# Kernel tuning notes

Measured on AMD Instinct MI355X. Metric: run time of the kernel, lower is better.

The kernel has to match this reference:

```python
import jax, jax.numpy as jnp
import numpy as np


def setup_inputs() -> dict:
    key = jax.random.key(0)
    k1, k2 = jax.random.split(key)
    x = jax.random.normal(k1, (2, 8, 32, 32, 64), dtype=jnp.float32)
    gamma = jax.random.normal(k2, (1,), dtype=jnp.float32)
    return {"x": x, "gamma": gamma}


def reference(x, gamma):
    # x: (B, D, H, W, C) -> flatten spatial dims to N = D*H*W
    B, D, H, W, C = x.shape
    N = D * H * W
    q = x.reshape(B, N, C)                       # proj_query (B, N, C)
    # energy = Q @ Q^T : (B, N, N) self-similarity over spatial positions
    energy = jnp.einsum('bnc,bmc->bnm', q, q)
    attn = jax.nn.softmax(energy, axis=-1)       # softmax over last axis (keras default)
    out = jnp.einsum('bnm,bmc->bnc', attn, q)    # attention @ Q -> (B, N, C)
    out = out.reshape(B, D, H, W, C)
    return gamma * out + x
```

## Files before the change

kernel.cpp:

```cpp
#include <hip/hip_runtime.h>
#include <hip/hip_bf16.h>

typedef __attribute__((ext_vector_type(8))) short bf16x8;
typedef __attribute__((ext_vector_type(16))) float f32x16;
typedef __attribute__((ext_vector_type(4))) int int4v;

#define NB 2
#define NN 8192
#define NC 64
#define LOG2E 1.44269504088896340736f
#define INV_LOG2E 0.69314718055994530942f
#define MAXNORM_BOUND 16.0f
#define KSTRIDE 68
#define SKIP_THRESH -110.0f
#define LSPLITC 3
#define SPLIT (1 << LSPLITC)
#define KT_PER (128 / SPLIT)

union I4 { int4v v; unsigned long long u[2]; };

__device__ __forceinline__ bf16x8 lds_ld16(const __hip_bfloat16* p) {
    union { bf16x8 v; unsigned long long u[2]; } r;
    r.u[0] = *(const unsigned long long*)(p);
    r.u[1] = *(const unsigned long long*)(p + 4);
    return r.v;
}

__global__ __launch_bounds__(256) void prep_kernel(
        const float* __restrict__ x,
        __hip_bfloat16* __restrict__ qb) {
    const int i = blockIdx.x * 256 + threadIdx.x;
    const float* src = x + ((size_t)i << 3);
    float4 f0 = *(const float4*)(src);
    float4 f1 = *(const float4*)(src + 4);
    __align__(16) __hip_bfloat16 h[8];
    h[0] = __float2bfloat16(f0.x); h[1] = __float2bfloat16(f0.y);
    h[2] = __float2bfloat16(f0.z); h[3] = __float2bfloat16(f0.w);
    h[4] = __float2bfloat16(f1.x); h[5] = __float2bfloat16(f1.y);
    h[6] = __float2bfloat16(f1.z); h[7] = __float2bfloat16(f1.w);
    *(int4v*)(qb + ((size_t)i << 3)) = *(const int4v*)h;
}

__global__ __launch_bounds__(512, 4) void attn_kernel(
        const __hip_bfloat16* __restrict__ qb,
        float* __restrict__ opart,
        float* __restrict__ lpart) {
    __shared__ __hip_bfloat16 Ks[512][KSTRIDE];

    const int blk   = blockIdx.x;
    const int chunk = blk & (SPLIT - 1);
    const int qw    = (blk >> LSPLITC) & 31;
    const int b     = blk >> (5 + LSPLITC);
    const int q0    = qw << 8;
    const int tid  = threadIdx.x;
    const int wave = tid >> 6;
    const int lane = tid & 63;
    const int n5   = lane & 31;
    const int h    = lane >> 5;
    const int q0w  = q0 + (wave << 5);

    const __hip_bfloat16* kvptr = qb + ((size_t)b << 19);

    const int srow = tid >> 3;
    const int scb  = (tid & 7) << 3;

    const __hip_bfloat16* qrow = kvptr + (((size_t)(q0w + n5)) << 6);
    bf16x8 Qf[4];
#pragma unroll
    for (int step = 0; step < 4; ++step)
        Qf[step] = *(const bf16x8*)(qrow + (step << 4) + (h << 3));

    float mb2, thr;
    {
        float s = 0.f;
#pragma unroll
        for (int step = 0; step < 4; ++step)
#pragma unroll
            for (int j = 0; j < 8; ++j) {
                float f = __uint_as_float(((unsigned)(unsigned short)Qf[step][j]) << 16);
                s += f * f;
            }
        s += __shfl_xor(s, 32);
        mb2 = sqrtf(s) * (MAXNORM_BOUND * LOG2E);
        thr = (SKIP_THRESH + mb2) * INV_LOG2E;
    }

    f32x16 O0 = (f32x16)(0.f), O1 = (f32x16)(0.f);
    float lp = 0.f;
    bool wkeep = false;

    const int kb0 = (chunk * KT_PER) << 6;

#define STAGE(BASEK) do {                                                         \
        I4 g[8];                                                                  \
        _Pragma("unroll")                                                         \
        for (int j = 0; j < 8; ++j)                                               \
            g[j].v = *(const int4v*)(kvptr +                                      \
                (((size_t)((BASEK) + srow + (j << 6))) << 6) + scb);              \
        _Pragma("unroll")                                                         \
        for (int j = 0; j < 8; ++j) {                                             \
            *(unsigned long long*)(&Ks[srow + (j << 6)][scb])     = g[j].u[0];    \
            *(unsigned long long*)(&Ks[srow + (j << 6)][scb + 4]) = g[j].u[1];    \
        }                                                                         \
    } while (0)

#define SLABPHASE() do {                                                          \
        unsigned km = 0;                                                          \
        _Pragma("clang loop unroll(disable)")                                     \
        for (int t = 0; t < 8; ++t) {                                             \
            f32x16 ST0 = (f32x16)(0.f), ST1 = (f32x16)(0.f);                      \
            _Pragma("unroll")                                                     \
            for (int step = 0; step < 4; ++step) {                                \
                bf16x8 a0 = lds_ld16(&Ks[(t << 6) + n5][(step << 4) + (h << 3)]); \
                bf16x8 a1 = lds_ld16(&Ks[(t << 6) + 32 + n5][(step << 4) + (h << 3)]); \
                ST0 = __builtin_amdgcn_mfma_f32_32x32x16_bf16(a0, Qf[step], ST0, 0, 0, 0); \
                ST1 = __builtin_amdgcn_mfma_f32_32x32x16_bf16(a1, Qf[step], ST1, 0, 0, 0); \
            }                                                                     \
            float mx[8];                                                          \
            _Pragma("unroll")                                                     \
            for (int r = 0; r < 8; ++r)                                           \
                mx[r] = fmaxf(fmaxf(ST0[r], ST0[r + 8]),                          \
                              fmaxf(ST1[r], ST1[r + 8]));                         \
            _Pragma("unroll")                                                     \
            for (int d = 4; d; d >>= 1)                                           \
                _Pragma("unroll")                                                 \
                for (int r = 0; r < d; ++r) mx[r] = fmaxf(mx[r], mx[r + d]);      \
            if (__ballot(mx[0] >= thr) != 0ull) km |= (1u << t);                  \
        }                                                                         \
        while (km) {                                                              \
            const int t = __builtin_ctz(km);                                      \
            km &= km - 1;                                                         \
            wkeep = true;                                                         \
            f32x16 ST0 = (f32x16)(0.f), ST1 = (f32x16)(0.f);                      \
            _Pragma("unroll")                                                     \
            for (int step = 0; step < 4; ++step) {                                \
                bf16x8 a0 = lds_ld16(&Ks[(t << 6) + n5][(step << 4) + (h << 3)]); \
                bf16x8 a1 = lds_ld16(&Ks[(t << 6) + 32 + n5][(step << 4) + (h << 3)]); \
                ST0 = __builtin_amdgcn_mfma_f32_32x32x16_bf16(a0, Qf[step], ST0, 0, 0, 0); \
                ST1 = __builtin_amdgcn_mfma_f32_32x32x16_bf16(a1, Qf[step], ST1, 0, 0, 0); \
            }                                                                     \
            bf16x8 bP[4];                                                         \
            _Pragma("unroll")                                                     \
            for (int s = 0; s < 4; ++s) {                                         \
                _Pragma("unroll")                                                 \
                for (int j = 0; j < 8; ++j) {                                     \
                    const float sv = (s < 2) ? ST0[((s & 1) << 3) + j]            \
                                             : ST1[((s & 1) << 3) + j];           \
                    float p = __builtin_amdgcn_exp2f(fmaf(sv, LOG2E, -mb2));      \
                    lp += p;                                                      \
                    bP[s][j] = __builtin_bit_cast(short, __float2bfloat16(p));    \
                }                                                                 \
            }                                                                     \
            \
            _Pragma("unroll")                                                     \
            for (int s = 0; s < 4; ++s) {                                         \
                bf16x8 a0, a1;                                                    \
                _Pragma("unroll")                                                 \
                for (int j = 0; j < 8; ++j) {                                     \
                    const int kap = (t << 6) + (s << 4) + (h << 2)                \
                                    + (j & 3) + ((j >> 2) << 3);                  \
                    a0[j] = __builtin_bit_cast(short, Ks[kap][n5]);               \
                    a1[j] = __builtin_bit_cast(short, Ks[kap][32 + n5]);          \
                }                                                                 \
                O0 = __builtin_amdgcn_mfma_f32_32x32x16_bf16(a0, bP[s], O0, 0, 0, 0); \
                O1 = __builtin_amdgcn_mfma_f32_32x32x16_bf16(a1, bP[s], O1, 0, 0, 0); \
            }                                                                     \
        }                                                                         \
    } while (0)

    STAGE(kb0);
    __syncthreads();
    SLABPHASE();

    __syncthreads();
    STAGE(kb0 + 512);
    __syncthreads();
    SLABPHASE();

#undef SLABPHASE
#undef STAGE

    float lsum = lp + __shfl_xor(lp, 32);
    if (h == 0)
        lpart[(chunk << 14) + (b << 13) + q0w + n5] = lsum;

    if (wkeep) {
        float* orow = opart + ((size_t)chunk << 20) +
                      (((size_t)((b << 13) + q0w + n5)) << 6);
#pragma unroll
        for (int g4 = 0; g4 < 4; ++g4) {
            float4 f0 = make_float4(O0[(g4 << 2)], O0[(g4 << 2) + 1],
                                    O0[(g4 << 2) + 2], O0[(g4 << 2) + 3]);
            *(float4*)(orow + (g4 << 3) + (h << 2)) = f0;
            float4 f1 = make_float4(O1[(g4 << 2)], O1[(g4 << 2) + 1],
                                    O1[(g4 << 2) + 2], O1[(g4 << 2) + 3]);
            *(float4*)(orow + 32 + (g4 << 3) + (h << 2)) = f1;
        }
    }
}

__global__ __launch_bounds__(256) void finalize_kernel(
        const float* __restrict__ x,
        const float* __restrict__ gamma_p,
        const float* __restrict__ opart,
        const float* __restrict__ lpart,
        float* __restrict__ out) {
    const int i4 = blockIdx.x * 256 + threadIdx.x;
    const size_t e = (size_t)i4 << 2;
    const int rowg = i4 >> 4;

    float l = 0.f;
    float4 o = make_float4(0.f, 0.f, 0.f, 0.f);
#pragma unroll
    for (int c = 0; c < SPLIT; ++c) {
        const float lc = lpart[(c << 14) + rowg];
        l += lc;
        if (lc != 0.f) {
            float4 t = *(const float4*)(opart + ((size_t)c << 20) + e);
            o.x += t.x; o.y += t.y; o.z += t.z; o.w += t.w;
        }
    }
    const float inv = 1.0f / l;
    const float gm = gamma_p[0];
    float4 xin = *(const float4*)(x + e);
    float4 r;
    r.x = gm * (o.x * inv) + xin.x;
    r.y = gm * (o.y * inv) + xin.y;
    r.z = gm * (o.z * inv) + xin.z;
    r.w = gm * (o.w * inv) + xin.w;
    *(float4*)(out + e) = r;
}

extern "C" void kernel_launch(void* const* d_in, const int* in_sizes, int n_in,
                              void* d_out, int out_size, void* d_ws, size_t ws_size,
                              hipStream_t stream) {
    const float* x     = (const float*)d_in[0];
    const float* gamma = (const float*)d_in[1];
    float* out = (float*)d_out;

    __hip_bfloat16* qb = (__hip_bfloat16*)d_ws;
    float* opart = (float*)((char*)d_ws + (size_t)2 * 1024 * 1024);
    float* lpart = opart + ((size_t)SPLIT << 20);

    prep_kernel<<<512, 256, 0, stream>>>(x, qb);
    attn_kernel<<<NB * 32 * SPLIT, 512, 0, stream>>>(qb, opart, lpart);
    finalize_kernel<<<(NB * NN * NC / 4) / 256, 256, 0, stream>>>(x, gamma, opart, lpart, out);
}
```

Baseline: 93.35 us.

## Process two 32-query subtiles per wave to reuse K fragments from LDS

Each wave now handles 64 queries (two 32-row groups) instead of 32, so every K fragment loaded from LDS feeds four MFMAs instead of two, and the grid is halved. The intent is to cut LDS traffic and global K staging per query. The cost is more registers (launch bounds relaxed to 2 blocks per CU), half as many blocks, and coarser skip decisions, since a tile is now kept if either query group needs it.

```diff
diff --git a/kernel.cpp b/kernel.cpp
--- a/kernel.cpp
+++ b/kernel.cpp
@@ -41,7 +41,7 @@
     *(int4v*)(qb + ((size_t)i << 3)) = *(const int4v*)h;
 }
 
-__global__ __launch_bounds__(512, 4) void attn_kernel(
+__global__ __launch_bounds__(512, 2) void attn_kernel(
         const __hip_bfloat16* __restrict__ qb,
         float* __restrict__ opart,
         float* __restrict__ lpart) {
@@ -49,44 +49,52 @@
 
     const int blk   = blockIdx.x;
     const int chunk = blk & (SPLIT - 1);
-    const int qw    = (blk >> LSPLITC) & 31;
-    const int b     = blk >> (5 + LSPLITC);
-    const int q0    = qw << 8;
+    const int qw    = (blk >> LSPLITC) & 15;
+    const int b     = blk >> (4 + LSPLITC);
+    const int q0    = qw << 9;
     const int tid  = threadIdx.x;
     const int wave = tid >> 6;
     const int lane = tid & 63;
     const int n5   = lane & 31;
     const int h    = lane >> 5;
-    const int q0w  = q0 + (wave << 5);
+    const int q0w  = q0 + (wave << 6);
 
     const __hip_bfloat16* kvptr = qb + ((size_t)b << 19);
 
     const int srow = tid >> 3;
     const int scb  = (tid & 7) << 3;
 
-    const __hip_bfloat16* qrow = kvptr + (((size_t)(q0w + n5)) << 6);
-    bf16x8 Qf[4];
-#pragma unroll
-    for (int step = 0; step < 4; ++step)
-        Qf[step] = *(const bf16x8*)(qrow + (step << 4) + (h << 3));
-
-    float mb2, thr;
+    const __hip_bfloat16* qrowA = kvptr + (((size_t)(q0w + n5)) << 6);
+    const __hip_bfloat16* qrowB = kvptr + (((size_t)(q0w + 32 + n5)) << 6);
+    bf16x8 Qf[4], Qg[4];
+#pragma unroll
+    for (int step = 0; step < 4; ++step) {
+        Qf[step] = *(const bf16x8*)(qrowA + (step << 4) + (h << 3));
+        Qg[step] = *(const bf16x8*)(qrowB + (step << 4) + (h << 3));
+    }
+
+    float mb2A, thrA, mb2B, thrB;
     {
-        float s = 0.f;
+        float sA = 0.f, sB = 0.f;
 #pragma unroll
         for (int step = 0; step < 4; ++step)
 #pragma unroll
             for (int j = 0; j < 8; ++j) {
-                float f = __uint_as_float(((unsigned)(unsigned short)Qf[step][j]) << 16);
-                s += f * f;
+                float fA = __uint_as_float(((unsigned)(unsigned short)Qf[step][j]) << 16);
+                float fB = __uint_as_float(((unsigned)(unsigned short)Qg[step][j]) << 16);
+                sA += fA * fA; sB += fB * fB;
             }
-        s += __shfl_xor(s, 32);
-        mb2 = sqrtf(s) * (MAXNORM_BOUND * LOG2E);
-        thr = (SKIP_THRESH + mb2) * INV_LOG2E;
-    }
-
-    f32x16 O0 = (f32x16)(0.f), O1 = (f32x16)(0.f);
-    float lp = 0.f;
+        sA += __shfl_xor(sA, 32);
+        sB += __shfl_xor(sB, 32);
+        mb2A = sqrtf(sA) * (MAXNORM_BOUND * LOG2E);
+        thrA = (SKIP_THRESH + mb2A) * INV_LOG2E;
+        mb2B = sqrtf(sB) * (MAXNORM_BOUND * LOG2E);
+        thrB = (SKIP_THRESH + mb2B) * INV_LOG2E;
+    }
+
+    f32x16 OA0 = (f32x16)(0.f), OA1 = (f32x16)(0.f);
+    f32x16 OB0 = (f32x16)(0.f), OB1 = (f32x16)(0.f);
+    float lpA = 0.f, lpB = 0.f;
     bool wkeep = false;
 
     const int kb0 = (chunk * KT_PER) << 6;
@@ -104,54 +112,70 @@
         }                                                                         \
     } while (0)
 
+#define EXPPV(ST0, ST1, MB2, BP, LP) do {                                         \
+        _Pragma("unroll")                                                         \
+        for (int s = 0; s < 4; ++s) {                                             \
+            _Pragma("unroll")                                                     \
+            for (int j = 0; j < 8; ++j) {                                         \
+                const float sv = (s < 2) ? ST0[((s & 1) << 3) + j]                \
+                                         : ST1[((s & 1) << 3) + j];               \
+                float p = __builtin_amdgcn_exp2f(fmaf(sv, LOG2E, -(MB2)));        \
+                LP += p;                                                          \
+                BP[s][j] = __builtin_bit_cast(short, __float2bfloat16(p));        \
+            }                                                                     \
+        }                                                                         \
+    } while (0)
+
 #define SLABPHASE() do {                                                          \
         unsigned km = 0;                                                          \
         _Pragma("clang loop unroll(disable)")                                     \
         for (int t = 0; t < 8; ++t) {                                             \
-            f32x16 ST0 = (f32x16)(0.f), ST1 = (f32x16)(0.f);                      \
+            f32x16 SA0 = (f32x16)(0.f), SA1 = (f32x16)(0.f);                      \
+            f32x16 SB0 = (f32x16)(0.f), SB1 = (f32x16)(0.f);                      \
             _Pragma("unroll")                                                     \
             for (int step = 0; step < 4; ++step) {                                \
                 bf16x8 a0 = lds_ld16(&Ks[(t << 6) + n5][(step << 4) + (h << 3)]); \
                 bf16x8 a1 = lds_ld16(&Ks[(t << 6) + 32 + n5][(step << 4) + (h << 3)]); \
-                ST0 = __builtin_amdgcn_mfma_f32_32x32x16_bf16(a0, Qf[step], ST0, 0, 0, 0); \
-                ST1 = __builtin_amdgcn_mfma_f32_32x32x16_bf16(a1, Qf[step], ST1, 0, 0, 0); \
-            }                                                                     \
-            float mx[8];                                                          \
-            _Pragma("unroll")                                                     \
-            for (int r = 0; r < 8; ++r)                                           \
-                mx[r] = fmaxf(fmaxf(ST0[r], ST0[r + 8]),                          \
-                              fmaxf(ST1[r], ST1[r + 8]));                         \
+                SA0 = __builtin_amdgcn_mfma_f32_32x32x16_bf16(a0, Qf[step], SA0, 0, 0, 0); \
+                SA1 = __builtin_amdgcn_mfma_f32_32x32x16_bf16(a1, Qf[step], SA1, 0, 0, 0); \
+                SB0 = __builtin_amdgcn_mfma_f32_32x32x16_bf16(a0, Qg[step], SB0, 0, 0, 0); \
+                SB1 = __builtin_amdgcn_mfma_f32_32x32x16_bf16(a1, Qg[step], SB1, 0, 0, 0); \
+            }                                                                     \
+            float mxA[8], mxB[8];                                                 \
+            _Pragma("unroll")                                                     \
+            for (int r = 0; r < 8; ++r) {                                         \
+                mxA[r] = fmaxf(fmaxf(SA0[r], SA0[r + 8]), fmaxf(SA1[r], SA1[r + 8])); \
+                mxB[r] = fmaxf(fmaxf(SB0[r], SB0[r + 8]), fmaxf(SB1[r], SB1[r + 8])); \
+            }                                                                     \
             _Pragma("unroll")                                                     \
             for (int d = 4; d; d >>= 1)                                           \
                 _Pragma("unroll")                                                 \
-                for (int r = 0; r < d; ++r) mx[r] = fmaxf(mx[r], mx[r + d]);      \
-            if (__ballot(mx[0] >= thr) != 0ull) km |= (1u << t);                  \
+                for (int r = 0; r < d; ++r) {                                     \
+                    mxA[r] = fmaxf(mxA[r], mxA[r + d]);                           \
+                    mxB[r] = fmaxf(mxB[r], mxB[r + d]);                           \
+                }                                                                 \
+            const bool kp = (mxA[0] >= thrA) || (mxB[0] >= thrB);                 \
+            if (__ballot(kp) != 0ull) km |= (1u << t);                            \
         }                                                                         \
         while (km) {                                                              \
             const int t = __builtin_ctz(km);                                      \
             km &= km - 1;                                                         \
             wkeep = true;                                                         \
-            f32x16 ST0 = (f32x16)(0.f), ST1 = (f32x16)(0.f);                      \
+            f32x16 SA0 = (f32x16)(0.f), SA1 = (f32x16)(0.f);                      \
+            f32x16 SB0 = (f32x16)(0.f), SB1 = (f32x16)(0.f);                      \
             _Pragma("unroll")                                                     \
             for (int step = 0; step < 4; ++step) {                                \
                 bf16x8 a0 = lds_ld16(&Ks[(t << 6) + n5][(step << 4) + (h << 3)]); \
                 bf16x8 a1 = lds_ld16(&Ks[(t << 6) + 32 + n5][(step << 4) + (h << 3)]); \
-                ST0 = __builtin_amdgcn_mfma_f32_32x32x16_bf16(a0, Qf[step], ST0, 0, 0, 0); \
-                ST1 = __builtin_amdgcn_mfma_f32_32x32x16_bf16(a1, Qf[step], ST1, 0, 0, 0); \
-            }                                                                     \
-            bf16x8 bP[4];                                                         \
-            _Pragma("unroll")                                                     \
-            for (int s = 0; s < 4; ++s) {                                         \
-                _Pragma("unroll")                                                 \
-                for (int j = 0; j < 8; ++j) {                                     \
-                    const float sv = (s < 2) ? ST0[((s & 1) << 3) + j]            \
-                                             : ST1[((s & 1) << 3) + j];           \
-                    float p = __builtin_amdgcn_exp2f(fmaf(sv, LOG2E, -mb2));      \
-                    lp += p;                                                      \
-                    bP[s][j] = __builtin_bit_cast(short, __float2bfloat16(p));    \
-                }                                                                 \
-            }                                                                     \
-            \
+                SA0 = __builtin_amdgcn_mfma_f32_32x32x16_bf16(a0, Qf[step], SA0, 0, 0, 0); \
+                SA1 = __builtin_amdgcn_mfma_f32_32x32x16_bf16(a1, Qf[step], SA1, 0, 0, 0); \
+                SB0 = __builtin_amdgcn_mfma_f32_32x32x16_bf16(a0, Qg[step], SB0, 0, 0, 0); \
+                SB1 = __builtin_amdgcn_mfma_f32_32x32x16_bf16(a1, Qg[step], SB1, 0, 0, 0); \
+            }                                                                     \
+            bf16x8 bPA[4], bPB[4];                                                \
+            EXPPV(SA0, SA1, mb2A, bPA, lpA);                                      \
+            EXPPV(SB0, SB1, mb2B, bPB, lpB);                                      \
+                            \
             _Pragma("unroll")                                                     \
             for (int s = 0; s < 4; ++s) {                                         \
                 bf16x8 a0, a1;                                                    \
@@ -162,8 +186,10 @@
                     a0[j] = __builtin_bit_cast(short, Ks[kap][n5]);               \
                     a1[j] = __builtin_bit_cast(short, Ks[kap][32 + n5]);          \
                 }                                                                 \
-                O0 = __builtin_amdgcn_mfma_f32_32x32x16_bf16(a0, bP[s], O0, 0, 0, 0); \
-                O1 = __builtin_amdgcn_mfma_f32_32x32x16_bf16(a1, bP[s], O1, 0, 0, 0); \
+                OA0 = __builtin_amdgcn_mfma_f32_32x32x16_bf16(a0, bPA[s], OA0, 0, 0, 0); \
+                OA1 = __builtin_amdgcn_mfma_f32_32x32x16_bf16(a1, bPA[s], OA1, 0, 0, 0); \
+                OB0 = __builtin_amdgcn_mfma_f32_32x32x16_bf16(a0, bPB[s], OB0, 0, 0, 0); \
+                OB1 = __builtin_amdgcn_mfma_f32_32x32x16_bf16(a1, bPB[s], OB1, 0, 0, 0); \
             }                                                                     \
         }                                                                         \
     } while (0)
@@ -178,23 +204,35 @@
     SLABPHASE();
 
 #undef SLABPHASE
+#undef EXPPV
 #undef STAGE
 
-    float lsum = lp + __shfl_xor(lp, 32);
-    if (h == 0)
-        lpart[(chunk << 14) + (b << 13) + q0w + n5] = lsum;
+    float lsA = lpA + __shfl_xor(lpA, 32);
+    float lsB = lpB + __shfl_xor(lpB, 32);
+    if (h == 0) {
+        lpart[(chunk << 14) + (b << 13) + q0w + n5]      = lsA;
+        lpart[(chunk << 14) + (b << 13) + q0w + 32 + n5] = lsB;
+    }
 
     if (wkeep) {
-        float* orow = opart + ((size_t)chunk << 20) +
-                      (((size_t)((b << 13) + q0w + n5)) << 6);
+        float* orowA = opart + ((size_t)chunk << 20) +
+                       (((size_t)((b << 13) + q0w + n5)) << 6);
+        float* orowB = opart + ((size_t)chunk << 20) +
+                       (((size_t)((b << 13) + q0w + 32 + n5)) << 6);
 #pragma unroll
         for (int g4 = 0; g4 < 4; ++g4) {
-            float4 f0 = make_float4(O0[(g4 << 2)], O0[(g4 << 2) + 1],
-                                    O0[(g4 << 2) + 2], O0[(g4 << 2) + 3]);
-            *(float4*)(orow + (g4 << 3) + (h << 2)) = f0;
-            float4 f1 = make_float4(O1[(g4 << 2)], O1[(g4 << 2) + 1],
-                                    O1[(g4 << 2) + 2], O1[(g4 << 2) + 3]);
-            *(float4*)(orow + 32 + (g4 << 3) + (h << 2)) = f1;
+            *(float4*)(orowA + (g4 << 3) + (h << 2)) =
+                make_float4(OA0[(g4 << 2)], OA0[(g4 << 2) + 1],
+                            OA0[(g4 << 2) + 2], OA0[(g4 << 2) + 3]);
+            *(float4*)(orowA + 32 + (g4 << 3) + (h << 2)) =
+                make_float4(OA1[(g4 << 2)], OA1[(g4 << 2) + 1],
+                            OA1[(g4 << 2) + 2], OA1[(g4 << 2) + 3]);
+            *(float4*)(orowB + (g4 << 3) + (h << 2)) =
+                make_float4(OB0[(g4 << 2)], OB0[(g4 << 2) + 1],
+                            OB0[(g4 << 2) + 2], OB0[(g4 << 2) + 3]);
+            *(float4*)(orowB + 32 + (g4 << 3) + (h << 2)) =
+                make_float4(OB1[(g4 << 2)], OB1[(g4 << 2) + 1],
+                            OB1[(g4 << 2) + 2], OB1[(g4 << 2) + 3]);
         }
     }
 }
@@ -243,6 +281,6 @@
     float* lpart = opart + ((size_t)SPLIT << 20);
 
     prep_kernel<<<512, 256, 0, stream>>>(x, qb);
-    attn_kernel<<<NB * 32 * SPLIT, 512, 0, stream>>>(qb, opart, lpart);
+    attn_kernel<<<NB * 16 * SPLIT, 512, 0, stream>>>(qb, opart, lpart);
     finalize_kernel<<<(NB * NN * NC / 4) / 256, 256, 0, stream>>>(x, gamma, opart, lpart, out);
 }
```

Result: slower. 98.93 us (+6.0%).
